# Optimization experiments

Measured on AMD Instinct MI355X. Metric: run time of the kernel, lower is better.

## Reference

```python
import jax, jax.numpy as jnp
import numpy as np

EMB = 128
EA = 32
ET = 32
N = 50000
E = 500000
EPS = 1e-5
DROP_P = 0.1


def setup_inputs() -> dict:
    key = jax.random.key(0)
    ks = jax.random.split(key, 12)
    din = EMB + EA + ET
    return {
        "hidden": jax.random.normal(ks[0], (N, EMB), jnp.float32),
        "edge_index": jax.random.randint(ks[1], (2, E), 0, N, jnp.int64 if jax.config.jax_enable_x64 else jnp.int32),
        "edge_attr": jax.random.normal(ks[2], (E, EA), jnp.float32),
        "edge_time_emb": jax.random.normal(ks[3], (E, ET), jnp.float32),
        "boundary_condition": jax.random.normal(ks[4], (N, EMB), jnp.float32),
        # learned params (torch Linear stored transposed: [in, out])
        "W_msg": jax.random.normal(ks[5], (din, EMB), jnp.float32) / np.sqrt(din),
        "b_msg": jnp.zeros((EMB,), jnp.float32),
        "W_lin": jax.random.normal(ks[6], (EMB, EMB), jnp.float32) / np.sqrt(EMB),
        "b_lin": jnp.zeros((EMB,), jnp.float32),
        "ln_gamma": jnp.ones((EMB,), jnp.float32),
        "ln_beta": jnp.zeros((EMB,), jnp.float32),
    }


def reference(hidden, edge_index, edge_attr, edge_time_emb, boundary_condition,
              W_msg, b_msg, W_lin, b_lin, ln_gamma, ln_beta):
    num_nodes = hidden.shape[0]
    # gather source node features, concat with edge features -> [E, emb+ea+et]
    msg = jnp.concatenate([hidden[edge_index[0]], edge_attr, edge_time_emb], axis=1)
    msg = jax.nn.relu(msg @ W_msg + b_msg)                      # [E, emb]
    # append boundary condition as self-loop messages
    msg_aug = jnp.concatenate([msg, boundary_condition], axis=0)
    idx_aug = jnp.concatenate([edge_index[1], jnp.arange(num_nodes, dtype=edge_index.dtype)])
    out = jax.ops.segment_sum(msg_aug, idx_aug, num_segments=num_nodes)  # scatter-sum [N, emb]
    out = out @ W_lin + b_lin
    # LayerNorm (eps=1e-5, affine)
    mean = out.mean(-1, keepdims=True)
    var = out.var(-1, keepdims=True)
    out = (out - mean) * jax.lax.rsqrt(var + EPS) * ln_gamma + ln_beta
    out = jax.nn.relu(out)
    # dropout p=0.1, training=True (fixed key for reproducibility)
    keep = jax.random.bernoulli(jax.random.key(42), 1.0 - DROP_P, out.shape)
    out = jnp.where(keep, out / (1.0 - DROP_P), 0.0)
    return out
```

## Files before the change

kernel.cpp:

```cpp
#include <hip/hip_runtime.h>
#include <stdint.h>

#define NN 50000
#define NE 500000
#define NEPAD 500032
#define SPB 64
#define NT_BLOCKS ((NN + 63) / 64)
#define DEG_STRIDE (NT_BLOCKS * 256)
#define NBLK_N ((NN + 255) / 256)

typedef short bf16x8 __attribute__((ext_vector_type(8)));
typedef float f32x4 __attribute__((ext_vector_type(4)));
typedef unsigned short u16;
typedef unsigned short u16x4 __attribute__((ext_vector_type(4)));
typedef unsigned short u16x8 __attribute__((ext_vector_type(8)));
typedef unsigned int u32x4 __attribute__((ext_vector_type(4)));

__device__ __forceinline__ u16 f2b(float x) {
  uint32_t u = __builtin_bit_cast(uint32_t, x);
  return (u16)((u + 0x7fffu + ((u >> 16) & 1u)) >> 16);
}
__device__ __forceinline__ float b2f(uint32_t lo16) {
  return __builtin_bit_cast(float, lo16 << 16);
}

__device__ __forceinline__ void threefry(uint32_t x0, uint32_t x1,
                                         uint32_t& o0, uint32_t& o1) {
  const uint32_t k0 = 0u, k1 = 42u, k2 = 0u ^ 42u ^ 0x1BD11BDAu;
  x0 += k0; x1 += k1;
#define TFR(r) { x0 += x1; x1 = (x1 << r) | (x1 >> (32 - r)); x1 ^= x0; }
  TFR(13) TFR(15) TFR(26) TFR(6)
  x0 += k1; x1 += k2 + 1u;
  TFR(17) TFR(29) TFR(16) TFR(24)
  x0 += k2; x1 += k0 + 2u;
  TFR(13) TFR(15) TFR(26) TFR(6)
  x0 += k0; x1 += k1 + 3u;
  TFR(17) TFR(29) TFR(16) TFR(24)
  x0 += k1; x1 += k2 + 4u;
  TFR(13) TFR(15) TFR(26) TFR(6)
  x0 += k2; x1 += k0 + 5u;
#undef TFR
  o0 = x0; o1 = x1;
}

__device__ __forceinline__ bool jax_keep(uint32_t j) {
  uint32_t o0, o1;
  threefry(0u, j, o0, o1);
  uint32_t bits = o0 ^ o1;
  float u = __builtin_bit_cast(float, (bits >> 9) | 0x3f800000u) - 1.0f;
  return u < 0.9f;
}

__global__ __launch_bounds__(256) void k_prep(const float* __restrict__ Wmsg,
                                              const float* __restrict__ Wlin,
                                              u16* __restrict__ WhImg,
                                              u16* __restrict__ WcImg,
                                              u16* __restrict__ WlImg) {
  const int t = threadIdx.x, b = blockIdx.x;
  if (b == 0) {
#pragma unroll
    for (int it = 0; it < 16; ++it) {
      int g = t + (it << 8);
      int d = g >> 5, k4 = (g & 31) << 2;
      u16x4 v = {f2b(Wmsg[(k4 + 0) * 128 + d]), f2b(Wmsg[(k4 + 1) * 128 + d]),
                 f2b(Wmsg[(k4 + 2) * 128 + d]), f2b(Wmsg[(k4 + 3) * 128 + d])};
      *(u16x4*)&WhImg[(d << 7) + k4] = v;
    }
  } else if (b == 1) {
#pragma unroll
    for (int it = 0; it < 8; ++it) {
      int g = t + (it << 8);
      int d = g >> 4, k4 = (g & 15) << 2;
      u16x4 v = {f2b(Wmsg[(128 + k4 + 0) * 128 + d]), f2b(Wmsg[(128 + k4 + 1) * 128 + d]),
                 f2b(Wmsg[(128 + k4 + 2) * 128 + d]), f2b(Wmsg[(128 + k4 + 3) * 128 + d])};
      *(u16x4*)&WcImg[(d << 6) + k4] = v;
    }
  } else {
#pragma unroll
    for (int it = 0; it < 16; ++it) {
      int g = t + (it << 8);
      int d = g >> 5, k4 = (g & 31) << 2;
      u16x4 v = {f2b(Wlin[(k4 + 0) * 128 + d]), f2b(Wlin[(k4 + 1) * 128 + d]),
                 f2b(Wlin[(k4 + 2) * 128 + d]), f2b(Wlin[(k4 + 3) * 128 + d])};
      *(u16x4*)&WlImg[(d << 7) + k4] = v;
    }
  }
}

__global__ __launch_bounds__(256) void k_scan1(const uint32_t* __restrict__ deg,
                                               uint32_t* __restrict__ ex,
                                               uint32_t* __restrict__ bsum) {
  __shared__ uint32_t s[256];
  int t = threadIdx.x;
  int i = blockIdx.x * 256 + t;
  uint32_t v = (i < NN) ? deg[i] : 0u;
  s[t] = v;
  __syncthreads();
#pragma unroll
  for (int off = 1; off < 256; off <<= 1) {
    uint32_t y = (t >= off) ? s[t - off] : 0u;
    __syncthreads();
    s[t] += y;
    __syncthreads();
  }
  if (i < NN) ex[i] = s[t] - v;
  if (t == 255) bsum[blockIdx.x] = s[255];
}

__global__ __launch_bounds__(256) void k_scan2(const uint32_t* __restrict__ bsum,
                                               uint32_t* __restrict__ boff) {
  __shared__ uint32_t s[256];
  int t = threadIdx.x;
  uint32_t v = (t < NBLK_N) ? bsum[t] : 0u;
  s[t] = v;
  __syncthreads();
#pragma unroll
  for (int off = 1; off < 256; off <<= 1) {
    uint32_t y = (t >= off) ? s[t - off] : 0u;
    __syncthreads();
    s[t] += y;
    __syncthreads();
  }
  boff[t] = s[t] - v;
}

__global__ __launch_bounds__(256) void k_scan3(const uint32_t* __restrict__ ex,
                                               const uint32_t* __restrict__ boff,
                                               uint32_t* __restrict__ cursor) {
  int i = blockIdx.x * 256 + threadIdx.x;
  if (i < NN) cursor[i] = ex[i] + boff[blockIdx.x];
}

__global__ __launch_bounds__(256) void k_perm(const int* __restrict__ ei,
                                              uint32_t* __restrict__ cursor,
                                              int* __restrict__ perm,
                                              uint32_t* __restrict__ sd) {
  int i = blockIdx.x * 256 + threadIdx.x;
  if (i < NE) {
    uint32_t s = (uint32_t)ei[i], d = (uint32_t)ei[NE + i];
    uint32_t pos = atomicAdd(&cursor[d], 1u);
    perm[pos] = i;
    sd[pos] = s | (d << 16);
  }
}

__global__ __launch_bounds__(256, 4) void k_edge3(const int* __restrict__ perm,
                                                  const uint32_t* __restrict__ sd,
                                                  const float* __restrict__ attr,
                                                  const float* __restrict__ tim,
                                                  const u16* __restrict__ WcImg,
                                                  const u16* __restrict__ Hp,
                                                  float* __restrict__ acc) {
  __shared__ union { u16 A[64 * 64]; float C[64 * 128]; } lds;
  __shared__ int sdst[64];
  const int t = threadIdx.x;
  const long e0 = (long)blockIdx.x << 6;

#pragma unroll
  for (int it = 0; it < 2; ++it) {
    int li = t + (it << 8);
    int row = li >> 3, g = li & 7;
    long sg = e0 + row;
    const bool vld = sg < NE;
    int e = 0;
    if (vld) e = perm[sg];
    const float* src8 = (g < 4) ? (attr + ((size_t)e << 5) + (g << 3))
                                : (tim + ((size_t)e << 5) + ((g - 4) << 3));
    f32x4 v0 = {0.f, 0.f, 0.f, 0.f}, v1 = {0.f, 0.f, 0.f, 0.f};
    if (vld) {
      v0 = *(const f32x4*)src8;
      v1 = *(const f32x4*)(src8 + 4);
    }
    u16x8 b = {f2b(v0[0]), f2b(v0[1]), f2b(v0[2]), f2b(v0[3]),
               f2b(v1[0]), f2b(v1[1]), f2b(v1[2]), f2b(v1[3])};
    *(u16x8*)&lds.A[(row << 6) + ((g ^ (row & 7)) << 3)] = b;
  }
  const int s = t >> 2, q = t & 3;
  const long sg1 = e0 + s;
  const bool v1 = sg1 < NE;
  int src = 0, dstn = -1;
  if (v1) {
    uint32_t sdv = sd[sg1];
    src = (int)(sdv & 0xffffu);
    dstn = (int)(sdv >> 16);
  }
  u32x4 hp[4];
  if (v1) {
    const u32x4* hp4 = (const u32x4*)(Hp + ((size_t)src << 7) + (q << 5));
#pragma unroll
    for (int g = 0; g < 4; ++g) hp[g] = hp4[g];
  }
  if (q == 0) sdst[s] = v1 ? dstn : -1;
  __syncthreads();

  const int lane = t & 63, w = t >> 6;
  const int quad = lane >> 4, lr = lane & 15;
  f32x4 c[4][2];
#pragma unroll
  for (int i = 0; i < 4; ++i)
#pragma unroll
    for (int j = 0; j < 2; ++j) { f32x4 z = {0.f, 0.f, 0.f, 0.f}; c[i][j] = z; }
#pragma unroll
  for (int ks = 0; ks < 64; ks += 32) {
    const int gi = (ks >> 3) + quad;
    bf16x8 a[4], b[2];
#pragma unroll
    for (int i = 0; i < 4; ++i) {
      int row = (i << 4) + lr;
      a[i] = *(const bf16x8*)&lds.A[(row << 6) + ((gi ^ (row & 7)) << 3)];
    }
#pragma unroll
    for (int j = 0; j < 2; ++j) {
      int col = (w << 5) + (j << 4) + lr;
      b[j] = *(const bf16x8*)&WcImg[(col << 6) + (gi << 3)];
    }
#pragma unroll
    for (int i = 0; i < 4; ++i)
#pragma unroll
      for (int j = 0; j < 2; ++j)
        c[i][j] = __builtin_amdgcn_mfma_f32_16x16x32_bf16(a[i], b[j], c[i][j], 0, 0, 0);
  }
  __syncthreads();
#pragma unroll
  for (int i = 0; i < 4; ++i)
#pragma unroll
    for (int j = 0; j < 2; ++j)
#pragma unroll
      for (int r = 0; r < 4; ++r) {
        int row = (i << 4) + (quad << 2) + r;
        int col = (w << 5) + (j << 4) + lr;
        lds.C[(row << 7) + ((((col >> 2) ^ (row & 31)) << 2) + (col & 3))] = c[i][j][r];
      }
  __syncthreads();
  if (v1) {
#pragma unroll
    for (int g = 0; g < 8; ++g) {
      int cb = (q << 5) + (g << 2);
      float* p = &lds.C[(s << 7) + ((((cb >> 2) ^ (s & 31)) << 2))];
      f32x4 cv = *(const f32x4*)p;
      uint32_t w0 = hp[g >> 1][(g & 1) << 1];
      uint32_t w1 = hp[g >> 1][((g & 1) << 1) + 1];
      cv[0] = fmaxf(cv[0] + b2f(w0 & 0xffffu), 0.f);
      cv[1] = fmaxf(cv[1] + b2f(w0 >> 16), 0.f);
      cv[2] = fmaxf(cv[2] + b2f(w1 & 0xffffu), 0.f);
      cv[3] = fmaxf(cv[3] + b2f(w1 >> 16), 0.f);
      *(f32x4*)p = cv;
    }
  }
  __syncthreads();
  {
    const int col = t & 127, half = t >> 7;
    const int beg = half << 5, end = beg + 32;
    int cur = sdst[beg];
    float sum = 0.f;
    int runstart = beg;
    for (int ss = beg; ss < end; ++ss) {
      int d = sdst[ss];
      if (d != cur) {
        if (cur >= 0) {
          float* p = acc + ((size_t)cur << 7) + col;
          if (runstart == beg) unsafeAtomicAdd(p, sum);
          else *p = sum;
        }
        cur = d; sum = 0.f; runstart = ss;
      }
      sum += lds.C[(ss << 7) + ((((col >> 2) ^ (ss & 31)) << 2) + (col & 3))];
    }
    if (cur >= 0) unsafeAtomicAdd(acc + ((size_t)cur << 7) + col, sum);
  }
}

__global__ __launch_bounds__(256) void k_hp(const float* __restrict__ hidden,
                                            const u16* __restrict__ WhImg,
                                            const float* __restrict__ bmsg,
                                            const int* __restrict__ ei,
                                            uint32_t* __restrict__ deg,
                                            u16* __restrict__ Hp) {
  __shared__ u16 sA[64 * 128];
  const int t = threadIdx.x;
  const int row0 = blockIdx.x << 6;
  for (int i = blockIdx.x * 256 + t; i < NE; i += DEG_STRIDE)
    atomicAdd(&deg[ei[NE + i]], 1u);
#pragma unroll
  for (int it = 0; it < 8; ++it) {
    int li = t + (it << 8);
    int row = li >> 5, c4 = li & 31;
    int n = row0 + row;
    f32x4 v = {0.f, 0.f, 0.f, 0.f};
    if (n < NN) v = *(const f32x4*)(hidden + ((size_t)n << 7) + (c4 << 2));
    u16x4 b = {f2b(v[0]), f2b(v[1]), f2b(v[2]), f2b(v[3])};
    *(u16x4*)&sA[(row << 7) + ((((c4 >> 1) ^ (row & 15)) << 3) + ((c4 & 1) << 2))] = b;
  }
  __syncthreads();
  const int lane = t & 63, w = t >> 6;
  const int quad = lane >> 4, lr = lane & 15;
  f32x4 c[4][2];
#pragma unroll
  for (int i = 0; i < 4; ++i)
#pragma unroll
    for (int j = 0; j < 2; ++j) { f32x4 z = {0.f, 0.f, 0.f, 0.f}; c[i][j] = z; }
#pragma unroll
  for (int ks = 0; ks < 128; ks += 32) {
    const int gi = (ks >> 3) + quad;
    bf16x8 a[4], b[2];
#pragma unroll
    for (int i = 0; i < 4; ++i) {
      int row = (i << 4) + lr;
      a[i] = *(const bf16x8*)&sA[(row << 7) + ((gi ^ (row & 15)) << 3)];
    }
#pragma unroll
    for (int j = 0; j < 2; ++j) {
      int col = (w << 5) + (j << 4) + lr;
      b[j] = *(const bf16x8*)&WhImg[(col << 7) + (gi << 3)];
    }
#pragma unroll
    for (int i = 0; i < 4; ++i)
#pragma unroll
      for (int j = 0; j < 2; ++j)
        c[i][j] = __builtin_amdgcn_mfma_f32_16x16x32_bf16(a[i], b[j], c[i][j], 0, 0, 0);
  }
#pragma unroll
  for (int j = 0; j < 2; ++j) {
    int d = (w << 5) + (j << 4) + lr;
    float bias = bmsg[d];
#pragma unroll
    for (int i = 0; i < 4; ++i) {
      int nb = row0 + (i << 4) + (quad << 2);
#pragma unroll
      for (int r = 0; r < 4; ++r) {
        int n = nb + r;
        if (n < NN) Hp[((size_t)n << 7) + d] = f2b(c[i][j][r] + bias);
      }
    }
  }
}

__global__ __launch_bounds__(256) void k_out(float* accout,
                                             const float* __restrict__ bnd,
                                             const u16* __restrict__ WlImg,
                                             const float* __restrict__ blin,
                                             const float* __restrict__ gam,
                                             const float* __restrict__ bet) {
  __shared__ union { u16 A[64 * 128]; float C[64 * 128]; } lds;
  const int t = threadIdx.x;
  const int row0 = blockIdx.x << 6;
#pragma unroll
  for (int it = 0; it < 8; ++it) {
    int li = t + (it << 8);
    int row = li >> 5, c4 = li & 31;
    int n = row0 + row;
    f32x4 v = {0.f, 0.f, 0.f, 0.f};
    if (n < NN) {
      f32x4 a = *(const f32x4*)(accout + ((size_t)n << 7) + (c4 << 2));
      f32x4 b = *(const f32x4*)(bnd + ((size_t)n << 7) + (c4 << 2));
      v = a + b;
    }
    u16x4 bb = {f2b(v[0]), f2b(v[1]), f2b(v[2]), f2b(v[3])};
    *(u16x4*)&lds.A[(row << 7) + ((((c4 >> 1) ^ (row & 15)) << 3) + ((c4 & 1) << 2))] = bb;
  }
  __syncthreads();
  const int lane = t & 63, w = t >> 6;
  const int quad = lane >> 4, lr = lane & 15;
  f32x4 c[4][2];
#pragma unroll
  for (int i = 0; i < 4; ++i)
#pragma unroll
    for (int j = 0; j < 2; ++j) { f32x4 z = {0.f, 0.f, 0.f, 0.f}; c[i][j] = z; }
#pragma unroll
  for (int ks = 0; ks < 128; ks += 32) {
    const int gi = (ks >> 3) + quad;
    bf16x8 a[4], b[2];
#pragma unroll
    for (int i = 0; i < 4; ++i) {
      int row = (i << 4) + lr;
      a[i] = *(const bf16x8*)&lds.A[(row << 7) + ((gi ^ (row & 15)) << 3)];
    }
#pragma unroll
    for (int j = 0; j < 2; ++j) {
      int col = (w << 5) + (j << 4) + lr;
      b[j] = *(const bf16x8*)&WlImg[(col << 7) + (gi << 3)];
    }
#pragma unroll
    for (int i = 0; i < 4; ++i)
#pragma unroll
      for (int j = 0; j < 2; ++j)
        c[i][j] = __builtin_amdgcn_mfma_f32_16x16x32_bf16(a[i], b[j], c[i][j], 0, 0, 0);
  }
  __syncthreads();
#pragma unroll
  for (int i = 0; i < 4; ++i)
#pragma unroll
    for (int j = 0; j < 2; ++j)
#pragma unroll
      for (int r = 0; r < 4; ++r) {
        int row = (i << 4) + (quad << 2) + r;
        int col = (w << 5) + (j << 4) + lr;
        lds.C[(row << 7) + ((((col >> 2) ^ (row & 31)) << 2) + (col & 3))] = c[i][j][r];
      }
  __syncthreads();
  const int row = t >> 2, q = t & 3;
  const int n = row0 + row;
  float s1 = 0.f, s2 = 0.f;
  if (n < NN) {
#pragma unroll
    for (int g = 0; g < 8; ++g) {
      int g5 = (q << 3) + g;
      f32x4 cv = *(const f32x4*)&lds.C[(row << 7) + ((g5 ^ (row & 31)) << 2)];
      f32x4 bl = *(const f32x4*)(blin + (g5 << 2));
#pragma unroll
      for (int m = 0; m < 4; ++m) {
        float x = cv[m] + bl[m];
        s1 += x; s2 += x * x;
      }
    }
  }
  s1 += __shfl_xor(s1, 1, 64); s1 += __shfl_xor(s1, 2, 64);
  s2 += __shfl_xor(s2, 1, 64); s2 += __shfl_xor(s2, 2, 64);
  if (n < NN) {
    const float mean = s1 * 0.0078125f;
    const float var = s2 * 0.0078125f - mean * mean;
    const float inv = 1.0f / sqrtf(var + 1e-5f);
#pragma unroll
    for (int g = 0; g < 8; ++g) {
      int g5 = (q << 3) + g;
      int d0 = g5 << 2;
      f32x4 cv = *(const f32x4*)&lds.C[(row << 7) + ((g5 ^ (row & 31)) << 2)];
      f32x4 bl = *(const f32x4*)(blin + d0);
      f32x4 gm = *(const f32x4*)(gam + d0);
      f32x4 bb = *(const f32x4*)(bet + d0);
      f32x4 o;
#pragma unroll
      for (int m = 0; m < 4; ++m) {
        float x = cv[m] + bl[m];
        float y = fmaxf((x - mean) * inv * gm[m] + bb[m], 0.f);
        uint32_t jj = ((uint32_t)n << 7) + (uint32_t)(d0 + m);
        o[m] = jax_keep(jj) ? (y * (1.0f / 0.9f)) : 0.0f;
      }
      *(f32x4*)(accout + ((size_t)n << 7) + d0) = o;
    }
  }
}

extern "C" void kernel_launch(void* const* d_in, const int* in_sizes, int n_in,
                              void* d_out, int out_size, void* d_ws, size_t ws_size,
                              hipStream_t stream) {
  (void)in_sizes; (void)n_in; (void)out_size; (void)ws_size;
  const float* hidden = (const float*)d_in[0];
  const int*   ei     = (const int*)d_in[1];
  const float* attr   = (const float*)d_in[2];
  const float* tim    = (const float*)d_in[3];
  const float* bnd    = (const float*)d_in[4];
  const float* Wmsg   = (const float*)d_in[5];
  const float* bmsg   = (const float*)d_in[6];
  const float* Wlin   = (const float*)d_in[7];
  const float* blin   = (const float*)d_in[8];
  const float* gam    = (const float*)d_in[9];
  const float* bet    = (const float*)d_in[10];

  float* acc = (float*)d_out;

  char* ws = (char*)d_ws;
  u16*      Hp     = (u16*)(ws + 0);
  u16*      WhImg  = (u16*)(ws + 12800000);
  u16*      WcImg  = (u16*)(ws + 12832768);
  u16*      WlImg  = (u16*)(ws + 12849152);
  uint32_t* deg    = (uint32_t*)(ws + 12881920);
  uint32_t* cursor = (uint32_t*)(ws + 13081920);
  uint32_t* bsum   = (uint32_t*)(ws + 13281920);
  uint32_t* boff   = (uint32_t*)(ws + 13282944);
  uint32_t* ex     = (uint32_t*)(ws + 13283968);
  uint32_t* sd     = (uint32_t*)(ws + 13483968);
  int*      perm   = (int*)(ws + 15484096);

  hipMemsetAsync(deg, 0, (size_t)NN * 4, stream);
  hipMemsetAsync(acc, 0, (size_t)NN * 128 * 4, stream);

  k_prep <<<dim3(3), dim3(256), 0, stream>>>(Wmsg, Wlin, WhImg, WcImg, WlImg);
  k_hp   <<<dim3(NT_BLOCKS), dim3(256), 0, stream>>>(hidden, WhImg, bmsg, ei, deg, Hp);
  k_scan1<<<dim3(NBLK_N), dim3(256), 0, stream>>>(deg, ex, bsum);
  k_scan2<<<dim3(1), dim3(256), 0, stream>>>(bsum, boff);
  k_scan3<<<dim3(NBLK_N), dim3(256), 0, stream>>>(ex, boff, cursor);
  k_perm <<<dim3((NE + 255) / 256), dim3(256), 0, stream>>>(ei, cursor, perm, sd);
  k_edge3<<<dim3(NEPAD / SPB), dim3(256), 0, stream>>>(perm, sd, attr, tim, WcImg, Hp, acc);
  k_out  <<<dim3(NT_BLOCKS), dim3(256), 0, stream>>>(acc, bnd, WlImg, blin, gam, bet);
}
```

Measured before the change: 362.3 us.

## Fold memsets and scan stages into kernels, halve edge tile, pack perm/sd

Removes both hipMemsetAsync calls by zeroing deg in extra k_prep blocks and acc inside k_hp. Merges scan2 and scan3 so each block redoes the small block-sum scan itself. Packs perm and src/dst into one 8-byte record per edge. Shrinks the edge tile from 64 to 32 edges with higher occupancy (launch bounds 8) and drops the padding checks, since 500000 divides evenly by 32. This cuts launch count and latency at the cost of more atomic flushes at block boundaries and redundant scan work.

```diff
diff --git a/kernel.cpp b/kernel.cpp
--- a/kernel.cpp
+++ b/kernel.cpp
@@ -3,8 +3,8 @@
 
 #define NN 50000
 #define NE 500000
-#define NEPAD 500032
-#define SPB 64
+#define SPB 32
+#define NEB (NE / SPB)
 #define NT_BLOCKS ((NN + 63) / 64)
 #define DEG_STRIDE (NT_BLOCKS * 256)
 #define NBLK_N ((NN + 255) / 256)
@@ -14,6 +14,7 @@
 typedef unsigned short u16;
 typedef unsigned short u16x4 __attribute__((ext_vector_type(4)));
 typedef unsigned short u16x8 __attribute__((ext_vector_type(8)));
+typedef unsigned int u32x2 __attribute__((ext_vector_type(2)));
 typedef unsigned int u32x4 __attribute__((ext_vector_type(4)));
 
 __device__ __forceinline__ u16 f2b(float x) {
@@ -55,7 +56,8 @@
                                               const float* __restrict__ Wlin,
                                               u16* __restrict__ WhImg,
                                               u16* __restrict__ WcImg,
-                                              u16* __restrict__ WlImg) {
+                                              u16* __restrict__ WlImg,
+                                              uint32_t* __restrict__ deg) {
   const int t = threadIdx.x, b = blockIdx.x;
   if (b == 0) {
 #pragma unroll
@@ -75,7 +77,7 @@
                  f2b(Wmsg[(128 + k4 + 2) * 128 + d]), f2b(Wmsg[(128 + k4 + 3) * 128 + d])};
       *(u16x4*)&WcImg[(d << 6) + k4] = v;
     }
-  } else {
+  } else if (b == 2) {
 #pragma unroll
     for (int it = 0; it < 16; ++it) {
       int g = t + (it << 8);
@@ -84,6 +86,8 @@
                  f2b(Wlin[(k4 + 2) * 128 + d]), f2b(Wlin[(k4 + 3) * 128 + d])};
       *(u16x4*)&WlImg[(d << 7) + k4] = v;
     }
+  } else {
+    for (int i = ((b - 3) << 8) + t; i < NN; i += 13 * 256) deg[i] = 0u;
   }
 }
 
@@ -107,8 +111,9 @@
   if (t == 255) bsum[blockIdx.x] = s[255];
 }
 
-__global__ __launch_bounds__(256) void k_scan2(const uint32_t* __restrict__ bsum,
-                                               uint32_t* __restrict__ boff) {
+__global__ __launch_bounds__(256) void k_scan23(const uint32_t* __restrict__ bsum,
+                                                const uint32_t* __restrict__ ex,
+                                                uint32_t* __restrict__ cursor) {
   __shared__ uint32_t s[256];
   int t = threadIdx.x;
   uint32_t v = (t < NBLK_N) ? bsum[t] : 0u;
@@ -121,93 +126,65 @@
     s[t] += y;
     __syncthreads();
   }
-  boff[t] = s[t] - v;
-}
-
-__global__ __launch_bounds__(256) void k_scan3(const uint32_t* __restrict__ ex,
-                                               const uint32_t* __restrict__ boff,
-                                               uint32_t* __restrict__ cursor) {
-  int i = blockIdx.x * 256 + threadIdx.x;
-  if (i < NN) cursor[i] = ex[i] + boff[blockIdx.x];
+  const uint32_t boff = s[blockIdx.x] - bsum[blockIdx.x];
+  int i = blockIdx.x * 256 + t;
+  if (i < NN) cursor[i] = ex[i] + boff;
 }
 
 __global__ __launch_bounds__(256) void k_perm(const int* __restrict__ ei,
                                               uint32_t* __restrict__ cursor,
-                                              int* __restrict__ perm,
-                                              uint32_t* __restrict__ sd) {
+                                              u32x2* __restrict__ psd) {
   int i = blockIdx.x * 256 + threadIdx.x;
   if (i < NE) {
     uint32_t s = (uint32_t)ei[i], d = (uint32_t)ei[NE + i];
     uint32_t pos = atomicAdd(&cursor[d], 1u);
-    perm[pos] = i;
-    sd[pos] = s | (d << 16);
-  }
-}
-
-__global__ __launch_bounds__(256, 4) void k_edge3(const int* __restrict__ perm,
-                                                  const uint32_t* __restrict__ sd,
+    u32x2 pv = {(uint32_t)i, s | (d << 16)};
+    psd[pos] = pv;
+  }
+}
+
+__global__ __launch_bounds__(256, 8) void k_edge3(const u32x2* __restrict__ psd,
                                                   const float* __restrict__ attr,
                                                   const float* __restrict__ tim,
                                                   const u16* __restrict__ WcImg,
                                                   const u16* __restrict__ Hp,
                                                   float* __restrict__ acc) {
-  __shared__ union { u16 A[64 * 64]; float C[64 * 128]; } lds;
-  __shared__ int sdst[64];
+  __shared__ union { u16 A[32 * 64]; float C[32 * 128]; } lds;
+  __shared__ int sdst[32];
   const int t = threadIdx.x;
-  const long e0 = (long)blockIdx.x << 6;
-
-#pragma unroll
-  for (int it = 0; it < 2; ++it) {
-    int li = t + (it << 8);
-    int row = li >> 3, g = li & 7;
-    long sg = e0 + row;
-    const bool vld = sg < NE;
-    int e = 0;
-    if (vld) e = perm[sg];
-    const float* src8 = (g < 4) ? (attr + ((size_t)e << 5) + (g << 3))
-                                : (tim + ((size_t)e << 5) + ((g - 4) << 3));
-    f32x4 v0 = {0.f, 0.f, 0.f, 0.f}, v1 = {0.f, 0.f, 0.f, 0.f};
-    if (vld) {
-      v0 = *(const f32x4*)src8;
-      v1 = *(const f32x4*)(src8 + 4);
-    }
-    u16x8 b = {f2b(v0[0]), f2b(v0[1]), f2b(v0[2]), f2b(v0[3]),
-               f2b(v1[0]), f2b(v1[1]), f2b(v1[2]), f2b(v1[3])};
-    *(u16x8*)&lds.A[(row << 6) + ((g ^ (row & 7)) << 3)] = b;
-  }
-  const int s = t >> 2, q = t & 3;
-  const long sg1 = e0 + s;
-  const bool v1 = sg1 < NE;
-  int src = 0, dstn = -1;
-  if (v1) {
-    uint32_t sdv = sd[sg1];
-    src = (int)(sdv & 0xffffu);
-    dstn = (int)(sdv >> 16);
-  }
-  u32x4 hp[4];
-  if (v1) {
-    const u32x4* hp4 = (const u32x4*)(Hp + ((size_t)src << 7) + (q << 5));
-#pragma unroll
-    for (int g = 0; g < 4; ++g) hp[g] = hp4[g];
-  }
-  if (q == 0) sdst[s] = v1 ? dstn : -1;
+  const long e0 = (long)blockIdx.x << 5;
+
+  const int row = t >> 3, g = t & 7;
+  const u32x2 pv = psd[e0 + row];
+  const int e = (int)pv.x;
+  const int src = (int)(pv.y & 0xffffu);
+  const float* src8 = (g < 4) ? (attr + ((size_t)e << 5) + (g << 3))
+                              : (tim + ((size_t)e << 5) + ((g - 4) << 3));
+  f32x4 v0 = *(const f32x4*)src8;
+  f32x4 v1 = *(const f32x4*)(src8 + 4);
+  u16x8 bb = {f2b(v0[0]), f2b(v0[1]), f2b(v0[2]), f2b(v0[3]),
+              f2b(v1[0]), f2b(v1[1]), f2b(v1[2]), f2b(v1[3])};
+  *(u16x8*)&lds.A[(row << 6) + ((g ^ (row & 7)) << 3)] = bb;
+  const u32x4 hpA = *(const u32x4*)(Hp + ((size_t)src << 7) + (g << 4));
+  const u32x4 hpB = *(const u32x4*)(Hp + ((size_t)src << 7) + (g << 4) + 8);
+  if (g == 0) sdst[row] = (int)(pv.y >> 16);
   __syncthreads();
 
   const int lane = t & 63, w = t >> 6;
   const int quad = lane >> 4, lr = lane & 15;
-  f32x4 c[4][2];
-#pragma unroll
-  for (int i = 0; i < 4; ++i)
+  f32x4 c[2][2];
+#pragma unroll
+  for (int i = 0; i < 2; ++i)
 #pragma unroll
     for (int j = 0; j < 2; ++j) { f32x4 z = {0.f, 0.f, 0.f, 0.f}; c[i][j] = z; }
 #pragma unroll
   for (int ks = 0; ks < 64; ks += 32) {
     const int gi = (ks >> 3) + quad;
-    bf16x8 a[4], b[2];
-#pragma unroll
-    for (int i = 0; i < 4; ++i) {
-      int row = (i << 4) + lr;
-      a[i] = *(const bf16x8*)&lds.A[(row << 6) + ((gi ^ (row & 7)) << 3)];
+    bf16x8 a[2], b[2];
+#pragma unroll
+    for (int i = 0; i < 2; ++i) {
+      int r2 = (i << 4) + lr;
+      a[i] = *(const bf16x8*)&lds.A[(r2 << 6) + ((gi ^ (r2 & 7)) << 3)];
     }
 #pragma unroll
     for (int j = 0; j < 2; ++j) {
@@ -215,31 +192,32 @@
       b[j] = *(const bf16x8*)&WcImg[(col << 6) + (gi << 3)];
     }
 #pragma unroll
-    for (int i = 0; i < 4; ++i)
+    for (int i = 0; i < 2; ++i)
 #pragma unroll
       for (int j = 0; j < 2; ++j)
         c[i][j] = __builtin_amdgcn_mfma_f32_16x16x32_bf16(a[i], b[j], c[i][j], 0, 0, 0);
   }
   __syncthreads();
 #pragma unroll
-  for (int i = 0; i < 4; ++i)
+  for (int i = 0; i < 2; ++i)
 #pragma unroll
     for (int j = 0; j < 2; ++j)
 #pragma unroll
       for (int r = 0; r < 4; ++r) {
-        int row = (i << 4) + (quad << 2) + r;
+        int rr = (i << 4) + (quad << 2) + r;
         int col = (w << 5) + (j << 4) + lr;
-        lds.C[(row << 7) + ((((col >> 2) ^ (row & 31)) << 2) + (col & 3))] = c[i][j][r];
-      }
-  __syncthreads();
-  if (v1) {
-#pragma unroll
-    for (int g = 0; g < 8; ++g) {
-      int cb = (q << 5) + (g << 2);
-      float* p = &lds.C[(s << 7) + ((((cb >> 2) ^ (s & 31)) << 2))];
+        lds.C[(rr << 7) + ((((col >> 2) ^ rr) << 2) + (col & 3))] = c[i][j][r];
+      }
+  __syncthreads();
+  {
+#pragma unroll
+    for (int gg = 0; gg < 4; ++gg) {
+      int cb4 = (g << 2) + gg;
+      float* p = &lds.C[(row << 7) + ((cb4 ^ row) << 2)];
       f32x4 cv = *(const f32x4*)p;
-      uint32_t w0 = hp[g >> 1][(g & 1) << 1];
-      uint32_t w1 = hp[g >> 1][((g & 1) << 1) + 1];
+      const u32x4 hw = (gg < 2) ? hpA : hpB;
+      const int k = (gg & 1) << 1;
+      uint32_t w0 = hw[k], w1 = hw[k + 1];
       cv[0] = fmaxf(cv[0] + b2f(w0 & 0xffffu), 0.f);
       cv[1] = fmaxf(cv[1] + b2f(w0 >> 16), 0.f);
       cv[2] = fmaxf(cv[2] + b2f(w1 & 0xffffu), 0.f);
@@ -250,7 +228,7 @@
   __syncthreads();
   {
     const int col = t & 127, half = t >> 7;
-    const int beg = half << 5, end = beg + 32;
+    const int beg = half << 4, end = beg + 16;
     int cur = sdst[beg];
     float sum = 0.f;
     int runstart = beg;
@@ -264,7 +242,7 @@
         }
         cur = d; sum = 0.f; runstart = ss;
       }
-      sum += lds.C[(ss << 7) + ((((col >> 2) ^ (ss & 31)) << 2) + (col & 3))];
+      sum += lds.C[(ss << 7) + ((((col >> 2) ^ ss) << 2) + (col & 3))];
     }
     if (cur >= 0) unsafeAtomicAdd(acc + ((size_t)cur << 7) + col, sum);
   }
@@ -275,10 +253,16 @@
                                             const float* __restrict__ bmsg,
                                             const int* __restrict__ ei,
                                             uint32_t* __restrict__ deg,
-                                            u16* __restrict__ Hp) {
+                                            u16* __restrict__ Hp,
+                                            float* __restrict__ acc) {
   __shared__ u16 sA[64 * 128];
   const int t = threadIdx.x;
   const int row0 = blockIdx.x << 6;
+  {
+    f32x4* acc4 = (f32x4*)acc;
+    const f32x4 z = {0.f, 0.f, 0.f, 0.f};
+    for (int i = blockIdx.x * 256 + t; i < NN * 32; i += DEG_STRIDE) acc4[i] = z;
+  }
   for (int i = blockIdx.x * 256 + t; i < NE; i += DEG_STRIDE)
     atomicAdd(&deg[ei[NE + i]], 1u);
 #pragma unroll
@@ -467,20 +451,14 @@
   uint32_t* deg    = (uint32_t*)(ws + 12881920);
   uint32_t* cursor = (uint32_t*)(ws + 13081920);
   uint32_t* bsum   = (uint32_t*)(ws + 13281920);
-  uint32_t* boff   = (uint32_t*)(ws + 13282944);
-  uint32_t* ex     = (uint32_t*)(ws + 13283968);
-  uint32_t* sd     = (uint32_t*)(ws + 13483968);
-  int*      perm   = (int*)(ws + 15484096);
-
-  hipMemsetAsync(deg, 0, (size_t)NN * 4, stream);
-  hipMemsetAsync(acc, 0, (size_t)NN * 128 * 4, stream);
-
-  k_prep <<<dim3(3), dim3(256), 0, stream>>>(Wmsg, Wlin, WhImg, WcImg, WlImg);
-  k_hp   <<<dim3(NT_BLOCKS), dim3(256), 0, stream>>>(hidden, WhImg, bmsg, ei, deg, Hp);
-  k_scan1<<<dim3(NBLK_N), dim3(256), 0, stream>>>(deg, ex, bsum);
-  k_scan2<<<dim3(1), dim3(256), 0, stream>>>(bsum, boff);
-  k_scan3<<<dim3(NBLK_N), dim3(256), 0, stream>>>(ex, boff, cursor);
-  k_perm <<<dim3((NE + 255) / 256), dim3(256), 0, stream>>>(ei, cursor, perm, sd);
-  k_edge3<<<dim3(NEPAD / SPB), dim3(256), 0, stream>>>(perm, sd, attr, tim, WcImg, Hp, acc);
-  k_out  <<<dim3(NT_BLOCKS), dim3(256), 0, stream>>>(acc, bnd, WlImg, blin, gam, bet);
-}
+  uint32_t* ex     = (uint32_t*)(ws + 13282944);
+  u32x2*    psd    = (u32x2*)(ws + 13482944);
+
+  k_prep  <<<dim3(16), dim3(256), 0, stream>>>(Wmsg, Wlin, WhImg, WcImg, WlImg, deg);
+  k_hp    <<<dim3(NT_BLOCKS), dim3(256), 0, stream>>>(hidden, WhImg, bmsg, ei, deg, Hp, acc);
+  k_scan1 <<<dim3(NBLK_N), dim3(256), 0, stream>>>(deg, ex, bsum);
+  k_scan23<<<dim3(NBLK_N), dim3(256), 0, stream>>>(bsum, ex, cursor);
+  k_perm  <<<dim3((NE + 255) / 256), dim3(256), 0, stream>>>(ei, cursor, psd);
+  k_edge3 <<<dim3(NEB), dim3(256), 0, stream>>>(psd, attr, tim, WcImg, Hp, acc);
+  k_out   <<<dim3(NT_BLOCKS), dim3(256), 0, stream>>>(acc, bnd, WlImg, blin, gam, bet);
+}
```

Result: faster. 332.7 us (-8.2%).
